# Optimization experiments

Measured on AMD Instinct MI355X. Metric: run time of the kernel, lower is better.

## Reference

```python
import jax, jax.numpy as jnp
import numpy as np

ALPHA = 3.0   # self.alpha
TAU = 0.1     # contrastive temperature
K = 8         # configs.k (top-k hyperedges per node)


def _scale(x, w, ehy, enod):
    """One scale of incidence_matrix_learn.
    x: [B, L, D] series tokens; w: [ws, D] word tokens;
    ehy: [H, D] hyperedge embedding table; enod: [N, D] node embedding table, N = L + ws.
    Returns (binary incidence matrix [N, H] float32, scalar contrastive loss).
    """
    B = x.shape[0]
    # concat_all[i]: cat(x.permute(0,2,1), word_expanded) -> [B, D, N]
    we = jnp.broadcast_to(w.T[None], (B,) + w.T.shape)          # [B, D, ws]
    concat = jnp.concatenate([jnp.transpose(x, (0, 2, 1)), we], axis=-1)  # [B, D, N]
    N, H = enod.shape[0], ehy.shape[0]
    # adjacency: softmax(relu(alpha * nodeec @ hyperen.T)) along hyperedge dim
    a = enod @ ehy.T                                            # [N, H]
    adj = jax.nn.softmax(jax.nn.relu(ALPHA * a), axis=-1)
    # top-k mask + threshold > 0.5 -> binary incidence matrix
    k = min(H, K)
    _, idx = jax.lax.top_k(adj, k)                              # [N, k]
    mask = jnp.zeros_like(adj).at[jnp.arange(N)[:, None], idx].set(1.0)
    adj_bin = ((adj * mask) > 0.5).astype(jnp.float32)          # [N, H]
    # positives: nodes sharing any hyperedge (build_pos_indices_from_edge_index),
    # equivalent to (A A^T > 0) with self excluded; dropping all-zero columns is a no-op here
    P = (adj_bin @ adj_bin.T > 0) & ~jnp.eye(N, dtype=bool)     # [N, N]
    cnt = P.sum(axis=1)                                         # positives per node
    # acl_loss_batched, vectorized over batch and nodes
    nodes = jnp.transpose(concat, (0, 2, 1))                    # [B, N, D]
    nrm = nodes / jnp.maximum(jnp.linalg.norm(nodes, axis=-1, keepdims=True), 1e-12)
    sim = jnp.einsum('bnd,bmd->bnm', nrm, nrm) / TAU            # [B, N, N]
    denom = jax.nn.logsumexp(sim, axis=-1)                      # [B, N]
    pos_mean = jnp.einsum('bnm,nm->bn', sim, P.astype(sim.dtype)) / jnp.maximum(cnt, 1)
    valid = cnt > 0                                             # [N]
    loss_sum = jnp.sum(jnp.where(valid[None, :], denom - pos_mean, 0.0))
    vc = B * valid.sum()
    loss = jnp.where(vc > 0, loss_sum / jnp.maximum(vc, 1), 0.0)
    return adj_bin, loss


def setup_inputs() -> dict:
    key = jax.random.key(0)
    ks = jax.random.split(key, 8)
    B, D = 64, 512
    return dict(
        x0=jax.random.normal(ks[0], (B, 512, D), dtype=jnp.float32),
        x1=jax.random.normal(ks[1], (B, 256, D), dtype=jnp.float32),
        word0=jax.random.normal(ks[2], (128, D), dtype=jnp.float32),
        word1=jax.random.normal(ks[3], (128, D), dtype=jnp.float32),
        embhy0=jax.random.normal(ks[4], (128, D), dtype=jnp.float32),
        embhy1=jax.random.normal(ks[5], (64, D), dtype=jnp.float32),
        embnod0=jax.random.normal(ks[6], (640, D), dtype=jnp.float32),
        embnod1=jax.random.normal(ks[7], (384, D), dtype=jnp.float32),
    )


def reference(x0, x1, word0, word1, embhy0, embhy1, embnod0, embnod1):
    a0, l0 = _scale(x0, word0, embhy0, embnod0)
    a1, l1 = _scale(x1, word1, embhy1, embnod1)
    return (a0, a1, l0 + l1)
```

## Files before the change

kernel.cpp:

```cpp
#include <hip/hip_runtime.h>


#define DDIM 512
#define BATCH 64

typedef __attribute__((ext_vector_type(8))) short short8;
typedef __attribute__((ext_vector_type(4))) float f32x4;

__device__ __forceinline__ unsigned short f2bf(float f) {
  unsigned int u = __float_as_uint(f);
  u += 0x7fffu + ((u >> 16) & 1u);
  return (unsigned short)(u >> 16);
}

__device__ __forceinline__ void async16(const void* g, void* l) {
  __builtin_amdgcn_global_load_lds(
      (const __attribute__((address_space(1))) unsigned int*)g,
      (__attribute__((address_space(3))) unsigned int*)l, 16, 0, 0);
}

__global__ __launch_bounds__(128) void adj_kernel(
    const float* __restrict__ enod0, const float* __restrict__ ehy0,
    const float* __restrict__ enod1, const float* __restrict__ ehy1,
    float* __restrict__ adj0, float* __restrict__ adj1,
    int* __restrict__ labels0, int* __restrict__ labels1,
    float* __restrict__ acc) {
  const int t = threadIdx.x;
  if (blockIdx.x == 0 && t == 0) { acc[0] = 0.f; acc[1] = 0.f; }
  const bool s0 = blockIdx.x < 640;
  const int n = s0 ? blockIdx.x : blockIdx.x - 640;
  const int H = s0 ? 128 : 64;
  const float* enod = s0 ? enod0 : enod1;
  const float* ehy = s0 ? ehy0 : ehy1;
  float* out_adj = s0 ? adj0 : adj1;
  int* labels = s0 ? labels0 : labels1;

  __shared__ float erow[DDIM];
  __shared__ float red[128];
  __shared__ int lab;
  ((float4*)erow)[t] = ((const float4*)(enod + (size_t)n * DDIM))[t];
  if (t == 0) lab = -1;
  __syncthreads();
  float v = 0.f;
  if (t < H) {
    const float4* hr = (const float4*)(ehy + (size_t)t * DDIM);
    float a = 0.f;
    #pragma unroll 8
    for (int d = 0; d < DDIM / 4; ++d) {
      float4 h = hr[d];
      float4 e = ((const float4*)erow)[d];
      a = fmaf(h.x, e.x, a); a = fmaf(h.y, e.y, a);
      a = fmaf(h.z, e.z, a); a = fmaf(h.w, e.w, a);
    }
    v = fmaxf(0.f, 3.0f * a);
  }
  red[t] = v;
  __syncthreads();
  for (int s = 64; s > 0; s >>= 1) {
    if (t < s) red[t] = fmaxf(red[t], red[t + s]);
    __syncthreads();
  }
  const float mx = red[0];
  __syncthreads();
  const float e = (t < H) ? __expf(v - mx) : 0.f;
  red[t] = e;
  __syncthreads();
  for (int s = 64; s > 0; s >>= 1) {
    if (t < s) red[t] += red[t + s];
    __syncthreads();
  }
  const float sum = red[0];
  if (t < H) {
    const float adj = e / sum;
    const float bin = (adj > 0.5f) ? 1.0f : 0.0f;
    out_adj[(size_t)n * H + t] = bin;
    if (bin > 0.f) lab = t;
  }
  __syncthreads();
  if (t == 0) labels[n] = lab;
}

__global__ __launch_bounds__(256) void cnt_kernel(
    const int* __restrict__ labels0, int* __restrict__ cnt0,
    const int* __restrict__ labels1, int* __restrict__ cnt1,
    int* __restrict__ valid) {
  const bool s0 = blockIdx.x == 0;
  const int* labels = s0 ? labels0 : labels1;
  int* cnt = s0 ? cnt0 : cnt1;
  int* validcnt = s0 ? valid : valid + 1;
  const int N = s0 ? 640 : 384;
  __shared__ int lab[640];
  __shared__ int hist[128];
  __shared__ int vc;
  const int t = threadIdx.x;
  if (t == 0) vc = 0;
  if (t < 128) hist[t] = 0;
  for (int i = t; i < N; i += 256) lab[i] = labels[i];
  __syncthreads();
  for (int i = t; i < N; i += 256)
    if (lab[i] >= 0) atomicAdd(&hist[lab[i]], 1);
  __syncthreads();
  int lv = 0;
  for (int i = t; i < N; i += 256) {
    const int c = (lab[i] >= 0) ? hist[lab[i]] - 1 : 0;
    cnt[i] = c;
    if (c > 0) ++lv;
  }
  if (lv > 0) atomicAdd(&vc, lv);
  __syncthreads();
  if (t == 0) *validcnt = vc;
}

__global__ __launch_bounds__(128) void normalize_kernel(
    const float* __restrict__ x0, const float* __restrict__ w0,
    const float* __restrict__ x1, const float* __restrict__ w1,
    unsigned short* __restrict__ nhat0, unsigned short* __restrict__ nhat1) {
  int bid = blockIdx.x;
  const bool s0 = bid < BATCH * 640;
  if (!s0) bid -= BATCH * 640;
  const int N = s0 ? 640 : 384;
  const int L = s0 ? 512 : 256;
  const float* x = s0 ? x0 : x1;
  const float* w = s0 ? w0 : w1;
  unsigned short* nhat = s0 ? nhat0 : nhat1;
  const int b = bid / N;
  const int n = bid - b * N;
  const int t = threadIdx.x;
  const float* src = (n < L) ? (x + ((size_t)b * L + n) * DDIM)
                             : (w + (size_t)(n - L) * DDIM);
  const float4 v = ((const float4*)src)[t];
  float ss = v.x * v.x + v.y * v.y + v.z * v.z + v.w * v.w;
  #pragma unroll
  for (int off = 32; off > 0; off >>= 1) ss += __shfl_down(ss, off);
  __shared__ float s2[2];
  if ((t & 63) == 0) s2[t >> 6] = ss;
  __syncthreads();
  const float rinv = 1.0f / fmaxf(sqrtf(s2[0] + s2[1]), 1e-12f);
  ushort4 o;
  o.x = f2bf(v.x * rinv);
  o.y = f2bf(v.y * rinv);
  o.z = f2bf(v.z * rinv);
  o.w = f2bf(v.w * rinv);
  ((ushort4*)(nhat + ((size_t)b * N + n) * DDIM))[t] = o;
}

__global__ __launch_bounds__(256, 3) void lse_kernel(
    const unsigned short* __restrict__ nhat0, const int* __restrict__ labels0,
    const int* __restrict__ cnt0, const unsigned short* __restrict__ nhat1,
    const int* __restrict__ labels1, const int* __restrict__ cnt1,
    float* __restrict__ loss_acc) {
  __shared__ short8 Bbuf[2][1024];
  __shared__ int labS[640];
  __shared__ float redS[64];
  __shared__ float redP[64];
  const int tid = threadIdx.x;
  const bool s0 = blockIdx.x < 640;
  const int i = s0 ? blockIdx.x : blockIdx.x - 640;
  const int N = s0 ? 640 : 384;
  const int ntiles = s0 ? 10 : 6;
  const unsigned short* nhat = s0 ? nhat0 : nhat1;
  const int* labels = s0 ? labels0 : labels1;
  const int* cnt = s0 ? cnt0 : cnt1;
  float* acc_out = s0 ? loss_acc : loss_acc + 1;
  const int b = i & 63;
  const int tn = i >> 6;
  const int n0 = tn * 64;
  const int wave = tid >> 6;
  const int lane = tid & 63;
  const int lrow = lane & 15;
  const int lq = lane >> 4;
  for (int t = tid; t < N; t += 256) labS[t] = labels[t];

  const size_t base = (size_t)b * N * DDIM;
  const int rw0 = n0 + wave * 16;
  const unsigned short* Aptr = nhat + base + (size_t)(rw0 + lrow) * DDIM + lq * 8;
  short8 a[16];
  #pragma unroll
  for (int ks = 0; ks < 16; ++ks) a[ks] = *(const short8*)(Aptr + ks * 32);

  const int f0 = wave * 4;
  #pragma unroll
  for (int fi = 0; fi < 4; ++fi) {
    const int f = f0 + fi;
    const int j = f >> 2, ks = f & 3;
    const unsigned short* g = nhat + base +
        (size_t)(j * 16 + lrow) * DDIM + ks * 32 + lq * 8;
    async16(g, &Bbuf[0][f * 64]);
  }
  __syncthreads();

  const int grow = rw0 + lq * 4;
  int labn[4];
  #pragma unroll
  for (int r = 0; r < 4; ++r) labn[r] = labS[grow + r];

  float se[4] = {0.f, 0.f, 0.f, 0.f};
  float pos[4] = {0.f, 0.f, 0.f, 0.f};
  const int nchunks = ntiles * 4;

  for (int mt = 0; mt < ntiles; ++mt) {
    f32x4 acc[4];
    #pragma unroll
    for (int j = 0; j < 4; ++j) acc[j] = (f32x4){0.f, 0.f, 0.f, 0.f};
    #pragma unroll
    for (int kc = 0; kc < 4; ++kc) {
      const int nc = mt * 4 + kc + 1;
      if (nc < nchunks) {
        const int mt2 = nc >> 2, kc2 = nc & 3;
        short8* dst = &Bbuf[(kc + 1) & 1][0];
        #pragma unroll
        for (int fi = 0; fi < 4; ++fi) {
          const int f = f0 + fi;
          const int j = f >> 2, ks = f & 3;
          const unsigned short* g = nhat + base +
              (size_t)(mt2 * 64 + j * 16 + lrow) * DDIM +
              kc2 * 128 + ks * 32 + lq * 8;
          async16(g, dst + f * 64);
        }
      }
      const short8* bb = &Bbuf[kc & 1][0];
      #pragma unroll
      for (int ks = 0; ks < 4; ++ks) {
        const short8 b0 = bb[(0 + ks) * 64 + lane];
        const short8 b1 = bb[(4 + ks) * 64 + lane];
        const short8 b2 = bb[(8 + ks) * 64 + lane];
        const short8 b3 = bb[(12 + ks) * 64 + lane];
        const short8 av = a[kc * 4 + ks];
        acc[0] = __builtin_amdgcn_mfma_f32_16x16x32_bf16(av, b0, acc[0], 0, 0, 0);
        acc[1] = __builtin_amdgcn_mfma_f32_16x16x32_bf16(av, b1, acc[1], 0, 0, 0);
        acc[2] = __builtin_amdgcn_mfma_f32_16x16x32_bf16(av, b2, acc[2], 0, 0, 0);
        acc[3] = __builtin_amdgcn_mfma_f32_16x16x32_bf16(av, b3, acc[3], 0, 0, 0);
      }
      __syncthreads();
    }
    const int m0 = mt * 64;
    #pragma unroll
    for (int j = 0; j < 4; ++j) {
      const int m = m0 + j * 16 + lrow;
      const int labm = labS[m];
      #pragma unroll
      for (int r = 0; r < 4; ++r) {
        const float sim = acc[j][r] * 10.0f;
        se[r] += __expf(sim - 10.0f);
        if (labn[r] >= 0 && labm == labn[r] && m != grow + r) pos[r] += sim;
      }
    }
  }

  #pragma unroll
  for (int off = 1; off <= 8; off <<= 1) {
    #pragma unroll
    for (int r = 0; r < 4; ++r) {
      se[r] += __shfl_xor(se[r], off);
      pos[r] += __shfl_xor(pos[r], off);
    }
  }
  if (lrow == 0) {
    #pragma unroll
    for (int r = 0; r < 4; ++r) {
      redS[wave * 16 + lq * 4 + r] = se[r];
      redP[wave * 16 + lq * 4 + r] = pos[r];
    }
  }
  __syncthreads();
  if (tid < 64) {
    const int c = cnt[n0 + tid];
    if (c > 0)
      atomicAdd(acc_out, (10.0f + logf(redS[tid])) - redP[tid] / (float)c);
  }
}

__global__ void final_kernel(const float* __restrict__ acc,
                             const int* __restrict__ valid,
                             float* __restrict__ out) {
  float l = 0.f;
  if (valid[0] > 0) l += acc[0] / (float)(BATCH * valid[0]);
  if (valid[1] > 0) l += acc[1] / (float)(BATCH * valid[1]);
  out[0] = l;
}

extern "C" void kernel_launch(void* const* d_in, const int* in_sizes, int n_in,
                              void* d_out, int out_size, void* d_ws,
                              size_t ws_size, hipStream_t stream) {
  const float* x0 = (const float*)d_in[0];
  const float* x1 = (const float*)d_in[1];
  const float* w0 = (const float*)d_in[2];
  const float* w1 = (const float*)d_in[3];
  const float* ehy0 = (const float*)d_in[4];
  const float* ehy1 = (const float*)d_in[5];
  const float* enod0 = (const float*)d_in[6];
  const float* enod1 = (const float*)d_in[7];

  float* out = (float*)d_out;
  float* adj0 = out;
  float* adj1 = out + 640 * 128;
  float* lossp = out + 640 * 128 + 384 * 64;

  unsigned short* nhat0 = (unsigned short*)d_ws;
  unsigned short* nhat1 = nhat0 + (size_t)BATCH * 640 * DDIM;
  int* ip = (int*)(nhat1 + (size_t)BATCH * 384 * DDIM);
  int* labels0 = ip;
  int* labels1 = labels0 + 640;
  int* cnt0 = labels1 + 384;
  int* cnt1 = cnt0 + 640;
  int* valid = cnt1 + 384;
  float* acc = (float*)(valid + 2);

  adj_kernel<<<1024, 128, 0, stream>>>(enod0, ehy0, enod1, ehy1, adj0, adj1,
                                       labels0, labels1, acc);
  cnt_kernel<<<2, 256, 0, stream>>>(labels0, cnt0, labels1, cnt1, valid);
  normalize_kernel<<<BATCH * (640 + 384), 128, 0, stream>>>(x0, w0, x1, w1,
                                                            nhat0, nhat1);
  lse_kernel<<<1024, 256, 0, stream>>>(nhat0, labels0, cnt0, nhat1, labels1,
                                       cnt1, acc);
  final_kernel<<<1, 1, 0, stream>>>(acc, valid, lossp);
}
```

Baseline: 264.1 us.

## Fuse adjacency and normalize kernels; give each lse wave two row tiles

The adjacency and normalization kernels are merged into one launch. Adjacency blocks come first, and the remaining blocks normalize one row per wave, with two float4 loads per lane and a shuffle-xor reduction that needs no LDS. The lse kernel drops to 128 threads (2 waves), each wave owning 32 rows. Each B fragment loaded from LDS now feeds two MFMAs, halving LDS reads per MFMA, at the cost of more VGPRs (two A-register arrays and doubled accumulators) and fewer waves per block to hide latency.

```diff
diff --git a/kernel.cpp b/kernel.cpp
--- a/kernel.cpp
+++ b/kernel.cpp
@@ -19,65 +19,100 @@
       (__attribute__((address_space(3))) unsigned int*)l, 16, 0, 0);
 }
 
-__global__ __launch_bounds__(128) void adj_kernel(
+__global__ __launch_bounds__(256) void prep_kernel(
     const float* __restrict__ enod0, const float* __restrict__ ehy0,
     const float* __restrict__ enod1, const float* __restrict__ ehy1,
     float* __restrict__ adj0, float* __restrict__ adj1,
     int* __restrict__ labels0, int* __restrict__ labels1,
+    const float* __restrict__ x0, const float* __restrict__ w0,
+    const float* __restrict__ x1, const float* __restrict__ w1,
+    unsigned short* __restrict__ nhat0, unsigned short* __restrict__ nhat1,
     float* __restrict__ acc) {
   const int t = threadIdx.x;
-  if (blockIdx.x == 0 && t == 0) { acc[0] = 0.f; acc[1] = 0.f; }
-  const bool s0 = blockIdx.x < 640;
-  const int n = s0 ? blockIdx.x : blockIdx.x - 640;
-  const int H = s0 ? 128 : 64;
-  const float* enod = s0 ? enod0 : enod1;
-  const float* ehy = s0 ? ehy0 : ehy1;
-  float* out_adj = s0 ? adj0 : adj1;
-  int* labels = s0 ? labels0 : labels1;
-
-  __shared__ float erow[DDIM];
-  __shared__ float red[128];
-  __shared__ int lab;
-  ((float4*)erow)[t] = ((const float4*)(enod + (size_t)n * DDIM))[t];
-  if (t == 0) lab = -1;
-  __syncthreads();
-  float v = 0.f;
-  if (t < H) {
-    const float4* hr = (const float4*)(ehy + (size_t)t * DDIM);
-    float a = 0.f;
-    #pragma unroll 8
-    for (int d = 0; d < DDIM / 4; ++d) {
-      float4 h = hr[d];
-      float4 e = ((const float4*)erow)[d];
-      a = fmaf(h.x, e.x, a); a = fmaf(h.y, e.y, a);
-      a = fmaf(h.z, e.z, a); a = fmaf(h.w, e.w, a);
-    }
-    v = fmaxf(0.f, 3.0f * a);
-  }
-  red[t] = v;
-  __syncthreads();
-  for (int s = 64; s > 0; s >>= 1) {
-    if (t < s) red[t] = fmaxf(red[t], red[t + s]);
-    __syncthreads();
-  }
-  const float mx = red[0];
-  __syncthreads();
-  const float e = (t < H) ? __expf(v - mx) : 0.f;
-  red[t] = e;
-  __syncthreads();
-  for (int s = 64; s > 0; s >>= 1) {
-    if (t < s) red[t] += red[t + s];
-    __syncthreads();
-  }
-  const float sum = red[0];
-  if (t < H) {
-    const float adj = e / sum;
-    const float bin = (adj > 0.5f) ? 1.0f : 0.0f;
-    out_adj[(size_t)n * H + t] = bin;
-    if (bin > 0.f) lab = t;
-  }
-  __syncthreads();
-  if (t == 0) labels[n] = lab;
+  if (blockIdx.x < 1024) {
+    if (blockIdx.x == 0 && t == 0) { acc[0] = 0.f; acc[1] = 0.f; }
+    const bool s0 = blockIdx.x < 640;
+    const int n = s0 ? blockIdx.x : blockIdx.x - 640;
+    const int H = s0 ? 128 : 64;
+    const float* enod = s0 ? enod0 : enod1;
+    const float* ehy = s0 ? ehy0 : ehy1;
+    float* out_adj = s0 ? adj0 : adj1;
+    int* labels = s0 ? labels0 : labels1;
+    __shared__ float erow[DDIM];
+    __shared__ float red[128];
+    __shared__ int lab;
+    if (t < 128) ((float4*)erow)[t] = ((const float4*)(enod + (size_t)n * DDIM))[t];
+    if (t == 0) lab = -1;
+    __syncthreads();
+    float v = 0.f;
+    if (t < H) {
+      const float4* hr = (const float4*)(ehy + (size_t)t * DDIM);
+      float a = 0.f;
+      #pragma unroll 8
+      for (int d = 0; d < DDIM / 4; ++d) {
+        float4 h = hr[d];
+        float4 e = ((const float4*)erow)[d];
+        a = fmaf(h.x, e.x, a); a = fmaf(h.y, e.y, a);
+        a = fmaf(h.z, e.z, a); a = fmaf(h.w, e.w, a);
+      }
+      v = fmaxf(0.f, 3.0f * a);
+    }
+    if (t < 128) red[t] = v;
+    __syncthreads();
+    for (int s = 64; s > 0; s >>= 1) {
+      if (t < s) red[t] = fmaxf(red[t], red[t + s]);
+      __syncthreads();
+    }
+    const float mx = red[0];
+    __syncthreads();
+    const float e = (t < H) ? __expf(v - mx) : 0.f;
+    if (t < 128) red[t] = e;
+    __syncthreads();
+    for (int s = 64; s > 0; s >>= 1) {
+      if (t < s) red[t] += red[t + s];
+      __syncthreads();
+    }
+    const float sum = red[0];
+    if (t < H) {
+      const float adj = e / sum;
+      const float bin = (adj > 0.5f) ? 1.0f : 0.0f;
+      out_adj[(size_t)n * H + t] = bin;
+      if (bin > 0.f) lab = t;
+    }
+    __syncthreads();
+    if (t == 0) labels[n] = lab;
+  } else {
+    const int wave = t >> 6;
+    const int lane = t & 63;
+    const int g = (blockIdx.x - 1024) * 4 + wave;
+    const bool s0 = g < BATCH * 640;
+    const int gg = s0 ? g : g - BATCH * 640;
+    const int N = s0 ? 640 : 384;
+    const int L = s0 ? 512 : 256;
+    const float* x = s0 ? x0 : x1;
+    const float* w = s0 ? w0 : w1;
+    unsigned short* nhat = s0 ? nhat0 : nhat1;
+    const int b = gg / N;
+    const int n = gg - b * N;
+    const float* src = (n < L) ? (x + ((size_t)b * L + n) * DDIM)
+                               : (w + (size_t)(n - L) * DDIM);
+    const float4* rowp = (const float4*)src;
+    const float4 v0 = rowp[lane];
+    const float4 v1 = rowp[lane + 64];
+    float ss = v0.x * v0.x + v0.y * v0.y + v0.z * v0.z + v0.w * v0.w +
+               v1.x * v1.x + v1.y * v1.y + v1.z * v1.z + v1.w * v1.w;
+    #pragma unroll
+    for (int off = 32; off > 0; off >>= 1) ss += __shfl_xor(ss, off);
+    const float rinv = 1.0f / fmaxf(sqrtf(ss), 1e-12f);
+    ushort4 o0, o1;
+    o0.x = f2bf(v0.x * rinv); o0.y = f2bf(v0.y * rinv);
+    o0.z = f2bf(v0.z * rinv); o0.w = f2bf(v0.w * rinv);
+    o1.x = f2bf(v1.x * rinv); o1.y = f2bf(v1.y * rinv);
+    o1.z = f2bf(v1.z * rinv); o1.w = f2bf(v1.w * rinv);
+    ushort4* op = (ushort4*)(nhat + ((size_t)b * N + n) * DDIM);
+    op[lane] = o0;
+    op[lane + 64] = o1;
+  }
 }
 
 __global__ __launch_bounds__(256) void cnt_kernel(
@@ -111,40 +146,7 @@
   if (t == 0) *validcnt = vc;
 }
 
-__global__ __launch_bounds__(128) void normalize_kernel(
-    const float* __restrict__ x0, const float* __restrict__ w0,
-    const float* __restrict__ x1, const float* __restrict__ w1,
-    unsigned short* __restrict__ nhat0, unsigned short* __restrict__ nhat1) {
-  int bid = blockIdx.x;
-  const bool s0 = bid < BATCH * 640;
-  if (!s0) bid -= BATCH * 640;
-  const int N = s0 ? 640 : 384;
-  const int L = s0 ? 512 : 256;
-  const float* x = s0 ? x0 : x1;
-  const float* w = s0 ? w0 : w1;
-  unsigned short* nhat = s0 ? nhat0 : nhat1;
-  const int b = bid / N;
-  const int n = bid - b * N;
-  const int t = threadIdx.x;
-  const float* src = (n < L) ? (x + ((size_t)b * L + n) * DDIM)
-                             : (w + (size_t)(n - L) * DDIM);
-  const float4 v = ((const float4*)src)[t];
-  float ss = v.x * v.x + v.y * v.y + v.z * v.z + v.w * v.w;
-  #pragma unroll
-  for (int off = 32; off > 0; off >>= 1) ss += __shfl_down(ss, off);
-  __shared__ float s2[2];
-  if ((t & 63) == 0) s2[t >> 6] = ss;
-  __syncthreads();
-  const float rinv = 1.0f / fmaxf(sqrtf(s2[0] + s2[1]), 1e-12f);
-  ushort4 o;
-  o.x = f2bf(v.x * rinv);
-  o.y = f2bf(v.y * rinv);
-  o.z = f2bf(v.z * rinv);
-  o.w = f2bf(v.w * rinv);
-  ((ushort4*)(nhat + ((size_t)b * N + n) * DDIM))[t] = o;
-}
-
-__global__ __launch_bounds__(256, 3) void lse_kernel(
+__global__ __launch_bounds__(128, 2) void lse_kernel(
     const unsigned short* __restrict__ nhat0, const int* __restrict__ labels0,
     const int* __restrict__ cnt0, const unsigned short* __restrict__ nhat1,
     const int* __restrict__ labels1, const int* __restrict__ cnt1,
@@ -169,18 +171,22 @@
   const int lane = tid & 63;
   const int lrow = lane & 15;
   const int lq = lane >> 4;
-  for (int t = tid; t < N; t += 256) labS[t] = labels[t];
+  for (int t = tid; t < N; t += 128) labS[t] = labels[t];
 
   const size_t base = (size_t)b * N * DDIM;
-  const int rw0 = n0 + wave * 16;
-  const unsigned short* Aptr = nhat + base + (size_t)(rw0 + lrow) * DDIM + lq * 8;
-  short8 a[16];
+  const int rw0 = n0 + wave * 32;
+  const unsigned short* Ap0 = nhat + base + (size_t)(rw0 + lrow) * DDIM + lq * 8;
+  const unsigned short* Ap1 = nhat + base + (size_t)(rw0 + 16 + lrow) * DDIM + lq * 8;
+  short8 a0[16], a1[16];
   #pragma unroll
-  for (int ks = 0; ks < 16; ++ks) a[ks] = *(const short8*)(Aptr + ks * 32);
-
-  const int f0 = wave * 4;
+  for (int ks = 0; ks < 16; ++ks) {
+    a0[ks] = *(const short8*)(Ap0 + ks * 32);
+    a1[ks] = *(const short8*)(Ap1 + ks * 32);
+  }
+
+  const int f0 = wave * 8;
   #pragma unroll
-  for (int fi = 0; fi < 4; ++fi) {
+  for (int fi = 0; fi < 8; ++fi) {
     const int f = f0 + fi;
     const int j = f >> 2, ks = f & 3;
     const unsigned short* g = nhat + base +
@@ -189,19 +195,23 @@
   }
   __syncthreads();
 
-  const int grow = rw0 + lq * 4;
-  int labn[4];
+  int labn[2][4];
   #pragma unroll
-  for (int r = 0; r < 4; ++r) labn[r] = labS[grow + r];
-
-  float se[4] = {0.f, 0.f, 0.f, 0.f};
-  float pos[4] = {0.f, 0.f, 0.f, 0.f};
+  for (int s = 0; s < 2; ++s)
+    #pragma unroll
+    for (int r = 0; r < 4; ++r) labn[s][r] = labS[rw0 + s * 16 + lq * 4 + r];
+
+  float se[2][4] = {{0.f, 0.f, 0.f, 0.f}, {0.f, 0.f, 0.f, 0.f}};
+  float pos[2][4] = {{0.f, 0.f, 0.f, 0.f}, {0.f, 0.f, 0.f, 0.f}};
   const int nchunks = ntiles * 4;
 
   for (int mt = 0; mt < ntiles; ++mt) {
-    f32x4 acc[4];
-    #pragma unroll
-    for (int j = 0; j < 4; ++j) acc[j] = (f32x4){0.f, 0.f, 0.f, 0.f};
+    f32x4 acc[4][2];
+    #pragma unroll
+    for (int j = 0; j < 4; ++j) {
+      acc[j][0] = (f32x4){0.f, 0.f, 0.f, 0.f};
+      acc[j][1] = (f32x4){0.f, 0.f, 0.f, 0.f};
+    }
     #pragma unroll
     for (int kc = 0; kc < 4; ++kc) {
       const int nc = mt * 4 + kc + 1;
@@ -209,7 +219,7 @@
         const int mt2 = nc >> 2, kc2 = nc & 3;
         short8* dst = &Bbuf[(kc + 1) & 1][0];
         #pragma unroll
-        for (int fi = 0; fi < 4; ++fi) {
+        for (int fi = 0; fi < 8; ++fi) {
           const int f = f0 + fi;
           const int j = f >> 2, ks = f & 3;
           const unsigned short* g = nhat + base +
@@ -225,11 +235,16 @@
         const short8 b1 = bb[(4 + ks) * 64 + lane];
         const short8 b2 = bb[(8 + ks) * 64 + lane];
         const short8 b3 = bb[(12 + ks) * 64 + lane];
-        const short8 av = a[kc * 4 + ks];
-        acc[0] = __builtin_amdgcn_mfma_f32_16x16x32_bf16(av, b0, acc[0], 0, 0, 0);
-        acc[1] = __builtin_amdgcn_mfma_f32_16x16x32_bf16(av, b1, acc[1], 0, 0, 0);
-        acc[2] = __builtin_amdgcn_mfma_f32_16x16x32_bf16(av, b2, acc[2], 0, 0, 0);
-        acc[3] = __builtin_amdgcn_mfma_f32_16x16x32_bf16(av, b3, acc[3], 0, 0, 0);
+        const short8 av0 = a0[kc * 4 + ks];
+        const short8 av1 = a1[kc * 4 + ks];
+        acc[0][0] = __builtin_amdgcn_mfma_f32_16x16x32_bf16(av0, b0, acc[0][0], 0, 0, 0);
+        acc[0][1] = __builtin_amdgcn_mfma_f32_16x16x32_bf16(av1, b0, acc[0][1], 0, 0, 0);
+        acc[1][0] = __builtin_amdgcn_mfma_f32_16x16x32_bf16(av0, b1, acc[1][0], 0, 0, 0);
+        acc[1][1] = __builtin_amdgcn_mfma_f32_16x16x32_bf16(av1, b1, acc[1][1], 0, 0, 0);
+        acc[2][0] = __builtin_amdgcn_mfma_f32_16x16x32_bf16(av0, b2, acc[2][0], 0, 0, 0);
+        acc[2][1] = __builtin_amdgcn_mfma_f32_16x16x32_bf16(av1, b2, acc[2][1], 0, 0, 0);
+        acc[3][0] = __builtin_amdgcn_mfma_f32_16x16x32_bf16(av0, b3, acc[3][0], 0, 0, 0);
+        acc[3][1] = __builtin_amdgcn_mfma_f32_16x16x32_bf16(av1, b3, acc[3][1], 0, 0, 0);
       }
       __syncthreads();
     }
@@ -239,10 +254,15 @@
       const int m = m0 + j * 16 + lrow;
       const int labm = labS[m];
       #pragma unroll
-      for (int r = 0; r < 4; ++r) {
-        const float sim = acc[j][r] * 10.0f;
-        se[r] += __expf(sim - 10.0f);
-        if (labn[r] >= 0 && labm == labn[r] && m != grow + r) pos[r] += sim;
+      for (int s = 0; s < 2; ++s) {
+        const int row0 = rw0 + s * 16 + lq * 4;
+        #pragma unroll
+        for (int r = 0; r < 4; ++r) {
+          const float sim = acc[j][s][r] * 10.0f;
+          se[s][r] += __expf(sim - 10.0f);
+          if (labn[s][r] >= 0 && labm == labn[s][r] && m != row0 + r)
+            pos[s][r] += sim;
+        }
       }
     }
   }
@@ -250,17 +270,21 @@
   #pragma unroll
   for (int off = 1; off <= 8; off <<= 1) {
     #pragma unroll
-    for (int r = 0; r < 4; ++r) {
-      se[r] += __shfl_xor(se[r], off);
-      pos[r] += __shfl_xor(pos[r], off);
-    }
+    for (int s = 0; s < 2; ++s)
+      #pragma unroll
+      for (int r = 0; r < 4; ++r) {
+        se[s][r] += __shfl_xor(se[s][r], off);
+        pos[s][r] += __shfl_xor(pos[s][r], off);
+      }
   }
   if (lrow == 0) {
     #pragma unroll
-    for (int r = 0; r < 4; ++r) {
-      redS[wave * 16 + lq * 4 + r] = se[r];
-      redP[wave * 16 + lq * 4 + r] = pos[r];
-    }
+    for (int s = 0; s < 2; ++s)
+      #pragma unroll
+      for (int r = 0; r < 4; ++r) {
+        redS[wave * 32 + s * 16 + lq * 4 + r] = se[s][r];
+        redP[wave * 32 + s * 16 + lq * 4 + r] = pos[s][r];
+      }
   }
   __syncthreads();
   if (tid < 64) {
@@ -306,12 +330,11 @@
   int* valid = cnt1 + 384;
   float* acc = (float*)(valid + 2);
 
-  adj_kernel<<<1024, 128, 0, stream>>>(enod0, ehy0, enod1, ehy1, adj0, adj1,
-                                       labels0, labels1, acc);
+  prep_kernel<<<1024 + 16384, 256, 0, stream>>>(
+      enod0, ehy0, enod1, ehy1, adj0, adj1, labels0, labels1,
+      x0, w0, x1, w1, nhat0, nhat1, acc);
   cnt_kernel<<<2, 256, 0, stream>>>(labels0, cnt0, labels1, cnt1, valid);
-  normalize_kernel<<<BATCH * (640 + 384), 128, 0, stream>>>(x0, w0, x1, w1,
-                                                            nhat0, nhat1);
-  lse_kernel<<<1024, 256, 0, stream>>>(nhat0, labels0, cnt0, nhat1, labels1,
+  lse_kernel<<<1024, 128, 0, stream>>>(nhat0, labels0, cnt0, nhat1, labels1,
                                        cnt1, acc);
   final_kernel<<<1, 1, 0, stream>>>(acc, valid, lossp);
 }
```

After: 246.8 us. 6.6% less time.
